# Optimization experiments

Measured on AMD Instinct MI355X. Metric: run time of the kernel, lower is better.

Reference implementation:

```python
import jax, jax.numpy as jnp
import numpy as np

PHI = 1.618033988749895  # golden ratio
LUT_SIZE = 4096
TWO_PI = 2.0 * float(np.pi)
_grid = np.arange(LUT_SIZE, dtype=np.float32) * (TWO_PI / LUT_SIZE)
SIN_TABLE = jnp.asarray(np.sin(_grid).astype(np.float32))
COS_TABLE = jnp.asarray(np.cos(_grid).astype(np.float32))


def lut_sin_cos(theta):
    """4096-entry sin/cos lookup table over [0, 2pi) with linear interpolation."""
    pos = theta * (LUT_SIZE / TWO_PI)
    i0 = jnp.floor(pos)
    frac = (pos - i0).astype(theta.dtype)
    idx0 = jnp.mod(i0.astype(jnp.int32), LUT_SIZE)
    idx1 = jnp.mod(idx0 + 1, LUT_SIZE)
    sin_v = SIN_TABLE[idx0] * (1.0 - frac) + SIN_TABLE[idx1] * frac
    cos_v = COS_TABLE[idx0] * (1.0 - frac) + COS_TABLE[idx1] * frac
    return sin_v, cos_v


def _forward(input_ids, emb, w_query, b_query, w_key, b_key, w_ctx, W_res, B_res, w_pr, w_pi, w_out):
    B, S = input_ids.shape
    D = emb.shape[1] // 2
    H, dh = w_query.shape
    e = emb[input_ids]                               # [B,S,2D]
    w_emb, b_emb = e[..., :D], e[..., D:]
    t_arr = jnp.arange(S, dtype=jnp.float32)

    # --- sequential euler-transform recurrence (the only truly serial part) ---
    def step(carry, xs):
        h_r, h_i = carry
        w_t, b_t, t = xs                             # [B,D],[B,D],scalar
        wl = 1.0 + jnp.abs(w_t)
        tp = t * PHI
        th_r = h_r / wl + b_t + tp
        th_i = h_i / wl + b_t + tp
        sr, cr = lut_sin_cos(th_r)
        si, ci = lut_sin_cos(th_i)
        nr = cr * ci - sr * si
        ni = cr * si + sr * ci
        return (nr, ni), nr + ni

    init = (jnp.zeros((B, D), dtype=emb.dtype), jnp.zeros((B, D), dtype=emb.dtype))
    xs = (jnp.swapaxes(w_emb, 0, 1), jnp.swapaxes(b_emb, 0, 1), t_arr)
    _, states = jax.lax.scan(step, init, xs)         # [S,B,D]
    states = jnp.swapaxes(states, 0, 1)              # [B,S,D] == cached_states

    # --- multi-head LUT sin/cos attention over strictly-previous cached states ---
    xp = states.reshape(B, S, H, dh)                 # per-head patches
    t_phi = t_arr * PHI                              # [S]
    th_q = xp / (1.0 + jnp.abs(w_query)) + b_query + t_phi[None, :, None, None]
    sq, cq = lut_sin_cos(th_q)
    q = jnp.concatenate([cq, sq], axis=-1)           # [B,S,H,2dh]
    th_k = xp / (1.0 + jnp.abs(w_key)) + b_key
    sk, ck = lut_sin_cos(th_k)
    k = jnp.concatenate([ck, sk], axis=-1)           # [B,S,H,2dh]
    scale = float(np.sqrt(2.0 * dh))
    scores = jnp.einsum('bthd,bshd->bhts', q, k) / scale
    mask = jnp.tril(jnp.ones((S, S), dtype=bool), k=-1)   # keys strictly before query
    scores = jnp.where(mask[None, None], scores, -1e30)
    weights = jax.nn.softmax(scores, axis=-1)
    context = jnp.einsum('bhts,bsd->btd', weights, states)   # heads summed
    has_ctx = (t_arr > 0).astype(states.dtype)[None, :, None]  # t=0 has no cache
    x = states + has_ctx * (context @ w_ctx.T)

    # --- resonant layer over num_neurons ---
    wl_res = 1.0 + jnp.abs(W_res)                    # [N,D]
    theta = x[:, :, None, :] / wl_res + B_res + t_phi[None, :, None, None]  # [B,S,N,D]
    s_t, c_t = lut_sin_cos(theta)
    cos_sum = c_t.sum(-1)                            # [B,S,N]
    sin_sum = s_t.sum(-1)
    x = x + jax.nn.silu(cos_sum @ w_pr.T + sin_sum @ w_pi.T)

    return x @ w_out.T                               # [B,S,V]


def setup_inputs() -> dict:
    key = jax.random.key(0)
    ks = jax.random.split(key, 12)
    B, S, V, D, H, N = 8, 512, 32000, 64, 4, 128
    dh = D // H
    return {
        'input_ids': jax.random.randint(ks[0], (B, S), 0, V),
        'emb': jax.random.normal(ks[1], (V, 2 * D), dtype=jnp.float32) * 0.02,
        'w_query': jax.random.normal(ks[2], (H, dh), dtype=jnp.float32) * 0.02,
        'b_query': jnp.zeros((H, dh), dtype=jnp.float32),
        'w_key': jax.random.normal(ks[3], (H, dh), dtype=jnp.float32) * 0.02,
        'b_key': jnp.zeros((H, dh), dtype=jnp.float32),
        'w_ctx': jax.random.normal(ks[4], (D, D), dtype=jnp.float32) * 0.02,
        'W_res': jax.random.normal(ks[5], (N, D), dtype=jnp.float32) * 0.02,
        'B_res': jnp.zeros((N, D), dtype=jnp.float32),
        'w_pr': jax.random.normal(ks[6], (D, N), dtype=jnp.float32) * 0.02,
        'w_pi': jax.random.normal(ks[7], (D, N), dtype=jnp.float32) * 0.02,
        'w_out': jax.random.normal(ks[8], (V, D), dtype=jnp.float32) * 0.02,
    }


def reference(input_ids, emb, w_query, b_query, w_key, b_key, w_ctx, W_res, B_res, w_pr, w_pi, w_out):
    return _forward(input_ids, emb, w_query, b_query, w_key, b_key, w_ctx, W_res, B_res, w_pr, w_pi, w_out)
```

## Files before the change

### kernel.cpp

```cpp
#include <hip/hip_runtime.h>
#include <hip/hip_bf16.h>
#include <math.h>

#define PHI_F     1.618033988749895f
#define LUT_N     4096
#define LUT_INV   651.8986469044033f
#define LUT_STEP  0.0015339807878856412f

#define B_  8
#define S_  512
#define D_  64
#define H_  4
#define DH_ 16
#define N_  128
#define V_  32000
#define R_  (B_ * S_)

typedef __attribute__((ext_vector_type(8))) short short8_t;
typedef __attribute__((ext_vector_type(4))) float f32x4;

__device__ __forceinline__ void lut2(const float2* __restrict__ sc,
                                     float th, float& s, float& c) {
    float pos = th * LUT_INV;
    float f0  = floorf(pos);
    float fr  = pos - f0;
    int   i0  = ((int)f0) & (LUT_N - 1);
    int   i1  = (i0 + 1) & (LUT_N - 1);
    float2 p0 = sc[i0];
    float2 p1 = sc[i1];
    float om  = 1.0f - fr;
    s = p0.x * om + p1.x * fr;
    c = p0.y * om + p1.y * fr;
}

__global__ void k_tables(float2* __restrict__ scT2, float4* __restrict__ scT4) {
    int i = blockIdx.x * blockDim.x + threadIdx.x;
    if (i < LUT_N) {
        float g = (float)i * LUT_STEP;
        float s = (float)sin((double)g);
        float c = (float)cos((double)g);
        scT2[i] = make_float2(s, c);
        *(float2*)&scT4[i] = make_float2(s, c);
        *(((float2*)&scT4[(i - 1) & (LUT_N - 1)]) + 1) = make_float2(s, c);
    }
}

__global__ __launch_bounds__(256) void k_fused0(
        const int* __restrict__ ids, const float* __restrict__ emb,
        const float* __restrict__ Wres, const float* __restrict__ Bres,
        const float* __restrict__ wpr, const float* __restrict__ wpi,
        const float* __restrict__ wout, const float4* __restrict__ scT4,
        float* __restrict__ states, __hip_bfloat16* __restrict__ wb,
        float2* __restrict__ ibres, float2* __restrict__ wpT) {
    int blk = blockIdx.x;
    int tid = threadIdx.x;
    if (blk >= 8) {
        if (blk < 2008) {
            int i = (blk - 8) * 256 + tid;
            float4 v = ((const float4*)wout)[i];
            union { __hip_bfloat16 h[4]; short4 s4; } u;
            u.h[0] = __float2bfloat16(v.x);
            u.h[1] = __float2bfloat16(v.y);
            u.h[2] = __float2bfloat16(v.z);
            u.h[3] = __float2bfloat16(v.w);
            *(short4*)(&wb[4 * (size_t)i]) = u.s4;
        } else {
            int idx = (blk - 2008) * 256 + tid;
            ibres[idx] = make_float2(1.0f / (1.0f + fabsf(Wres[idx])), Bres[idx]);
            int nn = idx >> 6, d = idx & 63;
            wpT[idx] = make_float2(wpr[d * N_ + nn], wpi[d * N_ + nn]);
        }
        return;
    }
    __shared__ float4 sc4[LUT_N];
    for (int i = tid; i < LUT_N; i += 256) sc4[i] = scT4[i];
    __syncthreads();
    if (tid >= 64) return;
    int d = tid, b = blk;
    const int* idp = ids + b * S_;
    float cw[8], cb[8];
#pragma unroll
    for (int j = 0; j < 8; ++j) {
        int id = idp[j];
        cw[j] = emb[(size_t)id * 128 + d];
        cb[j] = emb[(size_t)id * 128 + 64 + d];
    }
    float* outp = states + (size_t)b * S_ * D_ + d;
    float hr = 0.0f, hi = 0.0f;
    for (int tc = 0; tc < S_; tc += 8) {
        float nw[8], nb[8], res[8];
#pragma unroll
        for (int jj = 0; jj < 8; ++jj) {
            int id = idp[(tc + 8 + jj) & (S_ - 1)];
            nw[jj] = emb[(size_t)id * 128 + d];
            nb[jj] = emb[(size_t)id * 128 + 64 + d];
        }
#pragma unroll
        for (int jj = 0; jj < 8; ++jj) {
            int   t   = tc + jj;
            float wl  = 1.0f + fabsf(cw[jj]);
            float btv = cb[jj];
            float tp  = (float)t * PHI_F;
            float thr = hr / wl + btv + tp;
            float thi = hi / wl + btv + tp;
            float posr = thr * LUT_INV;
            float posi = thi * LUT_INV;
            float fr0 = floorf(posr), fi0 = floorf(posi);
            float frr = posr - fr0,   fri = posi - fi0;
            int   ir  = ((int)fr0) & (LUT_N - 1);
            int   ii  = ((int)fi0) & (LUT_N - 1);
            float4 pr = sc4[ir];
            float4 pi = sc4[ii];
            float omr = 1.0f - frr, omi = 1.0f - fri;
            float sr = pr.x * omr + pr.z * frr;
            float cr = pr.y * omr + pr.w * frr;
            float si = pi.x * omi + pi.z * fri;
            float ci = pi.y * omi + pi.w * fri;
            float nr = cr * ci - sr * si;
            float ni = cr * si + sr * ci;
            hr = nr; hi = ni;
            res[jj] = nr + ni;
        }
#pragma unroll
        for (int jj = 0; jj < 8; ++jj) outp[(tc + jj) * D_] = res[jj];
#pragma unroll
        for (int jj = 0; jj < 8; ++jj) { cw[jj] = nw[jj]; cb[jj] = nb[jj]; }
    }
}

__global__ __launch_bounds__(256) void k_qk(const float* __restrict__ states,
                                            const float* __restrict__ wq,
                                            const float* __restrict__ bq,
                                            const float* __restrict__ wk,
                                            const float* __restrict__ bk,
                                            const float2* __restrict__ scT,
                                            float* __restrict__ q,
                                            float* __restrict__ kT) {
    int idx = blockIdx.x * 256 + threadIdx.x;
    int j  = idx & (DH_ - 1);
    int h  = (idx >> 4) & (H_ - 1);
    int bt = idx >> 6;
    int t  = bt & (S_ - 1);
    int b  = bt >> 9;
    float xp = states[idx];
    float tp = (float)t * PHI_F;
    int   hj = h * DH_ + j;
    float thq = xp / (1.0f + fabsf(wq[hj])) + bq[hj] + tp;
    float thk = xp / (1.0f + fabsf(wk[hj])) + bk[hj];
    float sq, cq, sk, ck;
    lut2(scT, thq, sq, cq);
    lut2(scT, thk, sk, ck);
    int base = bt * (H_ * 2 * DH_) + h * (2 * DH_) + j;
    q[base] = cq; q[base + DH_] = sq;
    size_t kb = ((size_t)(b * H_ + h) * 32 + j) * S_ + t;
    kT[kb] = ck; kT[kb + 16 * S_] = sk;
}

#define TB_ 4
__global__ __launch_bounds__(256) void k_attn(const float* __restrict__ states,
                                              const float* __restrict__ q,
                                              const float* __restrict__ kT,
                                              const float* __restrict__ wctx,
                                              float* __restrict__ x) {
    __shared__ float ql[H_][TB_][2 * DH_];
    __shared__ float wlds[H_][TB_][S_];
    __shared__ float cpart[4][TB_][D_];
    __shared__ float ctx[TB_][D_];
    int blk = blockIdx.x;
    int b = blk >> 7, tile = blk & 127;
    int t0 = tile * TB_;
    int tid = threadIdx.x;
    int h = tid >> 6, l = tid & 63;
    if (l < 2 * DH_) {
#pragma unroll
        for (int tt = 0; tt < TB_; ++tt)
            ql[h][tt][l] = q[((b << 9) + t0 + tt) * 128 + h * 32 + l];
    }
    __syncthreads();

    const float* kTb = kT + (size_t)(b * H_ + h) * 32 * S_;
    float sc[8][TB_];
    float m[TB_];
#pragma unroll
    for (int tt = 0; tt < TB_; ++tt) m[tt] = -INFINITY;
#pragma unroll
    for (int jj = 0; jj < 8; ++jj) {
        int s = l + jj * 64;
        float a0 = 0.f, a1 = 0.f, a2 = 0.f, a3 = 0.f;
        if (s < t0 + TB_ - 1) {
#pragma unroll
            for (int c = 0; c < 32; ++c) {
                float kv = kTb[c * S_ + s];
                a0 = fmaf(kv, ql[h][0][c], a0);
                a1 = fmaf(kv, ql[h][1][c], a1);
                a2 = fmaf(kv, ql[h][2][c], a2);
                a3 = fmaf(kv, ql[h][3][c], a3);
            }
        }
        const float scale = 0.1767766952966369f;
        float v0 = (s < t0 + 0) ? a0 * scale : -INFINITY;
        float v1 = (s < t0 + 1) ? a1 * scale : -INFINITY;
        float v2 = (s < t0 + 2) ? a2 * scale : -INFINITY;
        float v3 = (s < t0 + 3) ? a3 * scale : -INFINITY;
        sc[jj][0] = v0; m[0] = fmaxf(m[0], v0);
        sc[jj][1] = v1; m[1] = fmaxf(m[1], v1);
        sc[jj][2] = v2; m[2] = fmaxf(m[2], v2);
        sc[jj][3] = v3; m[3] = fmaxf(m[3], v3);
    }
#pragma unroll
    for (int tt = 0; tt < TB_; ++tt)
        for (int o = 32; o; o >>= 1) m[tt] = fmaxf(m[tt], __shfl_xor(m[tt], o));
    float sum[TB_] = {0.f, 0.f, 0.f, 0.f};
#pragma unroll
    for (int jj = 0; jj < 8; ++jj)
#pragma unroll
        for (int tt = 0; tt < TB_; ++tt) {
            float e = __expf(sc[jj][tt] - m[tt]);
            sc[jj][tt] = e; sum[tt] += e;
        }
#pragma unroll
    for (int tt = 0; tt < TB_; ++tt)
        for (int o = 32; o; o >>= 1) sum[tt] += __shfl_xor(sum[tt], o);
#pragma unroll
    for (int tt = 0; tt < TB_; ++tt) {
        float inv = 1.0f / sum[tt];
#pragma unroll
        for (int jj = 0; jj < 8; ++jj)
            wlds[h][tt][l + jj * 64] = sc[jj][tt] * inv;
    }
    __syncthreads();
    {
        int p = tid >> 6, d = tid & 63;
        float ac[TB_] = {0.f, 0.f, 0.f, 0.f};
        for (int s = p; s < t0 + TB_ - 1; s += 4) {
            float sv = states[(((size_t)b << 9) + s) * D_ + d];
#pragma unroll
            for (int tt = 0; tt < TB_; ++tt) {
                float w4 = wlds[0][tt][s] + wlds[1][tt][s]
                         + wlds[2][tt][s] + wlds[3][tt][s];
                if (s < t0 + tt) ac[tt] += w4 * sv;
            }
        }
#pragma unroll
        for (int tt = 0; tt < TB_; ++tt) cpart[p][tt][d] = ac[tt];
    }
    __syncthreads();
    {
        int tt = tid >> 6, dd = tid & 63;
        ctx[tt][dd] = cpart[0][tt][dd] + cpart[1][tt][dd]
                    + cpart[2][tt][dd] + cpart[3][tt][dd];
    }
    __syncthreads();
    {
        int tt = tid >> 6, dd = tid & 63;
        int t  = t0 + tt;
        size_t row = ((size_t)b << 9) + t;
        float base = states[row * D_ + dd];
        float val  = base;
        if (t > 0) {
            float y = 0.0f;
            const float* wr = wctx + dd * D_;
            for (int k = 0; k < D_; ++k) y += ctx[tt][k] * wr[k];
            val = base + y;
        }
        x[row * D_ + dd] = val;
    }
}

__global__ __launch_bounds__(256) void k_resid(const float* __restrict__ x,
                                               const float2* __restrict__ ibres,
                                               const float2* __restrict__ wpT,
                                               const float2* __restrict__ scT,
                                               __hip_bfloat16* __restrict__ xb) {
    __shared__ float2 sc[LUT_N];
    __shared__ float xv8[8][D_];
    __shared__ float csum[N_], ssum[N_];
    __shared__ float part[4][D_];
    int tid = threadIdx.x;
    for (int i = tid; i < LUT_N; i += 256) sc[i] = scT[i];
    {
        int r2 = tid >> 5, o = tid & 31;
        size_t base = (size_t)(blockIdx.x * 8 + r2) * D_;
        xv8[r2][o]      = x[base + o];
        xv8[r2][o + 32] = x[base + o + 32];
    }
    int n  = tid >> 1;
    int d0 = (tid & 1) * 32;
    float2 ib[32];
#pragma unroll
    for (int dd = 0; dd < 32; ++dd) ib[dd] = ibres[n * D_ + d0 + dd];
    int g = tid >> 6, dl = tid & 63;
    __syncthreads();
    for (int r = 0; r < 8; ++r) {
        int bt = blockIdx.x * 8 + r;
        int t  = bt & (S_ - 1);
        float tp = (float)t * PHI_F;
        float cs = 0.0f, ss = 0.0f;
#pragma unroll
        for (int dd = 0; dd < 32; ++dd) {
            float th = fmaf(xv8[r][d0 + dd], ib[dd].x, ib[dd].y) + tp;
            float s, c;
            lut2(sc, th, s, c);
            cs += c; ss += s;
        }
        cs += __shfl_xor(cs, 1);
        ss += __shfl_xor(ss, 1);
        if ((tid & 1) == 0) { csum[n] = cs; ssum[n] = ss; }
        __syncthreads();
        float acc = 0.0f;
#pragma unroll
        for (int nn = 0; nn < 32; ++nn) {
            float2 w = wpT[(g * 32 + nn) * D_ + dl];
            acc = fmaf(csum[g * 32 + nn], w.x, fmaf(ssum[g * 32 + nn], w.y, acc));
        }
        part[g][dl] = acc;
        __syncthreads();
        if (tid < D_) {
            float pre = part[0][tid] + part[1][tid] + part[2][tid] + part[3][tid];
            float sig = 1.0f / (1.0f + __expf(-pre));
            xb[bt * D_ + tid] = __float2bfloat16(xv8[r][tid] + pre * sig);
        }
    }
}

__global__ __launch_bounds__(256) void k_out(const __hip_bfloat16* __restrict__ xb,
                                             const __hip_bfloat16* __restrict__ wb,
                                             float* __restrict__ out) {
    __shared__ float ot[64][132];
    int tid  = threadIdx.x;
    int wave = tid >> 6, l = tid & 63;
    int wr = wave >> 1, wc = wave & 1;
    int m0 = blockIdx.y * 64 + wr * 32;
    int r  = l & 15;
    int ks = (l >> 4) * 8;
    int kh = l >> 4;

    short8_t a[2][2];
#pragma unroll
    for (int mi = 0; mi < 2; ++mi)
#pragma unroll
        for (int kk = 0; kk < 2; ++kk)
            a[mi][kk] = *reinterpret_cast<const short8_t*>(
                xb + (size_t)(m0 + mi * 16 + r) * 64 + kk * 32 + ks);

    for (int ch = 0; ch < 2; ++ch) {
        int c0 = blockIdx.x * 256 + ch * 128 + wc * 64;
        short8_t b[4][2];
#pragma unroll
        for (int ni = 0; ni < 4; ++ni)
#pragma unroll
            for (int kk = 0; kk < 2; ++kk)
                b[ni][kk] = *reinterpret_cast<const short8_t*>(
                    wb + (size_t)(c0 + ni * 16 + r) * 64 + kk * 32 + ks);

        f32x4 acc[2][4];
#pragma unroll
        for (int mi = 0; mi < 2; ++mi)
#pragma unroll
            for (int ni = 0; ni < 4; ++ni) {
                acc[mi][ni] = (f32x4){0.f, 0.f, 0.f, 0.f};
                acc[mi][ni] = __builtin_amdgcn_mfma_f32_16x16x32_bf16(
                    a[mi][0], b[ni][0], acc[mi][ni], 0, 0, 0);
                acc[mi][ni] = __builtin_amdgcn_mfma_f32_16x16x32_bf16(
                    a[mi][1], b[ni][1], acc[mi][ni], 0, 0, 0);
            }

        if (ch) __syncthreads();
#pragma unroll
        for (int mi = 0; mi < 2; ++mi)
#pragma unroll
            for (int ni = 0; ni < 4; ++ni)
#pragma unroll
                for (int i = 0; i < 4; ++i)
                    ot[wr * 32 + mi * 16 + kh * 4 + i][wc * 64 + ni * 16 + r] = acc[mi][ni][i];
        __syncthreads();

        size_t rbase = blockIdx.y * 64;
        size_t cb    = (size_t)blockIdx.x * 256 + ch * 128;
#pragma unroll
        for (int j = 0; j < 8; ++j) {
            int idx = j * 256 + tid;
            int row = idx >> 5, c4 = idx & 31;
            f32x4 v = *(const f32x4*)&ot[row][c4 * 4];
            __builtin_nontemporal_store(v,
                (f32x4*)&out[(rbase + row) * V_ + cb + c4 * 4]);
        }
    }
}

extern "C" void kernel_launch(void* const* d_in, const int* in_sizes, int n_in,
                              void* d_out, int out_size, void* d_ws, size_t ws_size,
                              hipStream_t stream) {
    const int*   ids  = (const int*)  d_in[0];
    const float* emb  = (const float*)d_in[1];
    const float* wq   = (const float*)d_in[2];
    const float* bq   = (const float*)d_in[3];
    const float* wk   = (const float*)d_in[4];
    const float* bk   = (const float*)d_in[5];
    const float* wctx = (const float*)d_in[6];
    const float* Wres = (const float*)d_in[7];
    const float* Bres = (const float*)d_in[8];
    const float* wpr  = (const float*)d_in[9];
    const float* wpi  = (const float*)d_in[10];
    const float* wout = (const float*)d_in[11];
    float* out = (float*)d_out;

    float* states = (float*)d_ws;
    float* qbuf   = states + R_ * D_;
    float* kTbuf  = qbuf + R_ * 128;
    float* xbuf   = kTbuf + B_ * H_ * 32 * S_;
    __hip_bfloat16* wb = (__hip_bfloat16*)(xbuf + R_ * D_);
    __hip_bfloat16* xb = wb + (size_t)V_ * D_;
    float2* scT   = (float2*)(xb + R_ * D_);
    float2* ibres = scT + LUT_N;
    float2* wpT   = ibres + N_ * D_;
    float4* scT4  = (float4*)(wpT + N_ * D_);

    k_tables<<<16, 256, 0, stream>>>(scT, scT4);
    k_fused0<<<2040, 256, 0, stream>>>(ids, emb, Wres, Bres, wpr, wpi, wout, scT4,
                                       states, wb, ibres, wpT);
    k_qk    <<<1024, 256, 0, stream>>>(states, wq, bq, wk, bk, scT, qbuf, kTbuf);
    k_attn  <<<1024, 256, 0, stream>>>(states, qbuf, kTbuf, wctx, xbuf);
    k_resid <<<R_ / 8, 256, 0, stream>>>(xbuf, ibres, wpT, scT, xb);
    k_out   <<<dim3(V_ / 256, R_ / 64), 256, 0, stream>>>(xb, wb, out);
}
```

Measured before the change: 321.3 us.

## Drop LDS LUT staging in resid kernel and retile output GEMM as persistent row-strips

```diff
diff --git a/kernel.cpp b/kernel.cpp
--- a/kernel.cpp
+++ b/kernel.cpp
@@ -270,19 +270,15 @@
 __global__ __launch_bounds__(256) void k_resid(const float* __restrict__ x,
                                                const float2* __restrict__ ibres,
                                                const float2* __restrict__ wpT,
-                                               const float2* __restrict__ scT,
+                                               const float4* __restrict__ scT4,
                                                __hip_bfloat16* __restrict__ xb) {
-    __shared__ float2 sc[LUT_N];
-    __shared__ float xv8[8][D_];
+    __shared__ float xv[4][D_];
     __shared__ float csum[N_], ssum[N_];
     __shared__ float part[4][D_];
     int tid = threadIdx.x;
-    for (int i = tid; i < LUT_N; i += 256) sc[i] = scT[i];
     {
-        int r2 = tid >> 5, o = tid & 31;
-        size_t base = (size_t)(blockIdx.x * 8 + r2) * D_;
-        xv8[r2][o]      = x[base + o];
-        xv8[r2][o + 32] = x[base + o + 32];
+        int r2 = tid >> 6, o = tid & 63;
+        xv[r2][o] = x[(size_t)(blockIdx.x * 4 + r2) * D_ + o];
     }
     int n  = tid >> 1;
     int d0 = (tid & 1) * 32;
@@ -291,16 +287,22 @@
     for (int dd = 0; dd < 32; ++dd) ib[dd] = ibres[n * D_ + d0 + dd];
     int g = tid >> 6, dl = tid & 63;
     __syncthreads();
-    for (int r = 0; r < 8; ++r) {
-        int bt = blockIdx.x * 8 + r;
+    for (int r = 0; r < 4; ++r) {
+        int bt = blockIdx.x * 4 + r;
         int t  = bt & (S_ - 1);
         float tp = (float)t * PHI_F;
         float cs = 0.0f, ss = 0.0f;
 #pragma unroll
         for (int dd = 0; dd < 32; ++dd) {
-            float th = fmaf(xv8[r][d0 + dd], ib[dd].x, ib[dd].y) + tp;
-            float s, c;
-            lut2(sc, th, s, c);
+            float th  = fmaf(xv[r][d0 + dd], ib[dd].x, ib[dd].y) + tp;
+            float pos = th * LUT_INV;
+            float f0  = floorf(pos);
+            float fr  = pos - f0;
+            int   i0  = ((int)f0) & (LUT_N - 1);
+            float4 p  = scT4[i0];
+            float om  = 1.0f - fr;
+            float s = p.x * om + p.z * fr;
+            float c = p.y * om + p.w * fr;
             cs += c; ss += s;
         }
         cs += __shfl_xor(cs, 1);
@@ -318,7 +320,7 @@
         if (tid < D_) {
             float pre = part[0][tid] + part[1][tid] + part[2][tid] + part[3][tid];
             float sig = 1.0f / (1.0f + __expf(-pre));
-            xb[bt * D_ + tid] = __float2bfloat16(xv8[r][tid] + pre * sig);
+            xb[bt * D_ + tid] = __float2bfloat16(xv[r][tid] + pre * sig);
         }
     }
 }
@@ -326,61 +328,59 @@
 __global__ __launch_bounds__(256) void k_out(const __hip_bfloat16* __restrict__ xb,
                                              const __hip_bfloat16* __restrict__ wb,
                                              float* __restrict__ out) {
-    __shared__ float ot[64][132];
+    __shared__ float ot[32][260];
+    int bid = blockIdx.x;
+    int rp  = bid / 5;
+    int sl  = bid % 5;
     int tid  = threadIdx.x;
     int wave = tid >> 6, l = tid & 63;
     int wr = wave >> 1, wc = wave & 1;
-    int m0 = blockIdx.y * 64 + wr * 32;
+    int m0 = rp * 32 + wr * 16;
     int r  = l & 15;
     int ks = (l >> 4) * 8;
     int kh = l >> 4;
 
-    short8_t a[2][2];
-#pragma unroll
-    for (int mi = 0; mi < 2; ++mi)
-#pragma unroll
-        for (int kk = 0; kk < 2; ++kk)
-            a[mi][kk] = *reinterpret_cast<const short8_t*>(
-                xb + (size_t)(m0 + mi * 16 + r) * 64 + kk * 32 + ks);
-
-    for (int ch = 0; ch < 2; ++ch) {
-        int c0 = blockIdx.x * 256 + ch * 128 + wc * 64;
-        short8_t b[4][2];
-#pragma unroll
-        for (int ni = 0; ni < 4; ++ni)
+    short8_t a[2];
+#pragma unroll
+    for (int kk = 0; kk < 2; ++kk)
+        a[kk] = *reinterpret_cast<const short8_t*>(
+            xb + (size_t)(m0 + r) * 64 + kk * 32 + ks);
+
+    size_t colbase = (size_t)sl * 6400;
+    for (int chk = 0; chk < 25; ++chk) {
+        int c0 = (int)colbase + chk * 256 + wc * 128;
+        short8_t b[8][2];
+#pragma unroll
+        for (int ni = 0; ni < 8; ++ni)
 #pragma unroll
             for (int kk = 0; kk < 2; ++kk)
                 b[ni][kk] = *reinterpret_cast<const short8_t*>(
                     wb + (size_t)(c0 + ni * 16 + r) * 64 + kk * 32 + ks);
 
-        f32x4 acc[2][4];
-#pragma unroll
-        for (int mi = 0; mi < 2; ++mi)
-#pragma unroll
-            for (int ni = 0; ni < 4; ++ni) {
-                acc[mi][ni] = (f32x4){0.f, 0.f, 0.f, 0.f};
-                acc[mi][ni] = __builtin_amdgcn_mfma_f32_16x16x32_bf16(
-                    a[mi][0], b[ni][0], acc[mi][ni], 0, 0, 0);
-                acc[mi][ni] = __builtin_amdgcn_mfma_f32_16x16x32_bf16(
-                    a[mi][1], b[ni][1], acc[mi][ni], 0, 0, 0);
-            }
-
-        if (ch) __syncthreads();
-#pragma unroll
-        for (int mi = 0; mi < 2; ++mi)
-#pragma unroll
-            for (int ni = 0; ni < 4; ++ni)
-#pragma unroll
-                for (int i = 0; i < 4; ++i)
-                    ot[wr * 32 + mi * 16 + kh * 4 + i][wc * 64 + ni * 16 + r] = acc[mi][ni][i];
+        f32x4 acc[8];
+#pragma unroll
+        for (int ni = 0; ni < 8; ++ni) {
+            acc[ni] = (f32x4){0.f, 0.f, 0.f, 0.f};
+            acc[ni] = __builtin_amdgcn_mfma_f32_16x16x32_bf16(
+                a[0], b[ni][0], acc[ni], 0, 0, 0);
+            acc[ni] = __builtin_amdgcn_mfma_f32_16x16x32_bf16(
+                a[1], b[ni][1], acc[ni], 0, 0, 0);
+        }
+
+        if (chk) __syncthreads();
+#pragma unroll
+        for (int ni = 0; ni < 8; ++ni)
+#pragma unroll
+            for (int i = 0; i < 4; ++i)
+                ot[wr * 16 + kh * 4 + i][wc * 128 + ni * 16 + r] = acc[ni][i];
         __syncthreads();
 
-        size_t rbase = blockIdx.y * 64;
-        size_t cb    = (size_t)blockIdx.x * 256 + ch * 128;
+        size_t rbase = (size_t)rp * 32;
+        size_t cb    = colbase + (size_t)chk * 256;
 #pragma unroll
         for (int j = 0; j < 8; ++j) {
             int idx = j * 256 + tid;
-            int row = idx >> 5, c4 = idx & 31;
+            int row = idx >> 6, c4 = idx & 63;
             f32x4 v = *(const f32x4*)&ot[row][c4 * 4];
             __builtin_nontemporal_store(v,
                 (f32x4*)&out[(rbase + row) * V_ + cb + c4 * 4]);
@@ -421,6 +421,6 @@
                                        states, wb, ibres, wpT);
     k_qk    <<<1024, 256, 0, stream>>>(states, wq, bq, wk, bk, scT, qbuf, kTbuf);
     k_attn  <<<1024, 256, 0, stream>>>(states, qbuf, kTbuf, wctx, xbuf);
-    k_resid <<<R_ / 8, 256, 0, stream>>>(xbuf, ibres, wpT, scT, xb);
-    k_out   <<<dim3(V_ / 256, R_ / 64), 256, 0, stream>>>(xb, wb, out);
-}
+    k_resid <<<R_ / 4, 256, 0, stream>>>(xbuf, ibres, wpT, scT4, xb);
+    k_out   <<<640, 256, 0, stream>>>(xb, wb, out);
+}
```

After: 390.3 us. 21.5% more time.
